# Optimization experiments

Measured on AMD Instinct MI355X. Metric: run time of the kernel, lower is better.

Reference implementation:

```python
import jax, jax.numpy as jnp
import numpy as np

HEAD_DIM = 64
N_HEADS = 32
N_KV_HEADS = 8
ROPE_THETA = 10000.0


def _rotate_half(x):
    h = x.shape[-1] // 2
    return jnp.concatenate([-x[..., h:], x[..., :h]], axis=-1)


def _rope_cos_sin(position_ids, head_dim, theta, dtype):
    # position_ids: [b, s] int
    inv_freq = 1.0 / (theta ** (jnp.arange(0, head_dim, 2, dtype=jnp.float32) / head_dim))
    freqs = position_ids.astype(jnp.float32)[..., None] * inv_freq  # [b, s, hd/2]
    emb = jnp.concatenate([freqs, freqs], axis=-1)                  # [b, s, hd]
    return jnp.cos(emb).astype(dtype), jnp.sin(emb).astype(dtype)


def setup_inputs() -> dict:
    key = jax.random.key(0)
    ks = jax.random.split(key, 5)
    B, S, H = 2, 2048, 2048
    KVD = N_KV_HEADS * HEAD_DIM
    x = jax.random.normal(ks[0], (B, S, H), dtype=jnp.float32)
    position_ids = jnp.broadcast_to(jnp.arange(S, dtype=jnp.int64), (B, S))
    # additive causal mask: 0 on/below diagonal, -1e9 above
    causal = jnp.triu(jnp.full((S, S), -1e9, dtype=jnp.float32), k=1)
    mask = causal[None, None, :, :]
    sc = 1.0 / np.sqrt(H)
    wq = jax.random.normal(ks[1], (H, H), dtype=jnp.float32) * sc
    wk = jax.random.normal(ks[2], (KVD, H), dtype=jnp.float32) * sc
    wv = jax.random.normal(ks[3], (KVD, H), dtype=jnp.float32) * sc
    wo = jax.random.normal(ks[4], (H, H), dtype=jnp.float32) * sc
    return {"x": x, "position_ids": position_ids, "mask": mask,
            "wq": wq, "wk": wk, "wv": wv, "wo": wo}


def reference(x, position_ids, mask, wq, wk, wv, wo):
    b, s, h = x.shape
    kv_groups = N_HEADS // N_KV_HEADS
    # projections (Linear with weight [out, in])
    xq = jnp.einsum('bsh,oh->bso', x, wq)
    xk = jnp.einsum('bsh,oh->bso', x, wk)
    xv = jnp.einsum('bsh,oh->bso', x, wv)
    q = xq.reshape(b, s, N_HEADS, HEAD_DIM).transpose(0, 2, 1, 3)      # [b,H,s,d]
    k = xk.reshape(b, s, N_KV_HEADS, HEAD_DIM).transpose(0, 2, 1, 3)   # [b,Hk,s,d]
    v = xv.reshape(b, s, N_KV_HEADS, HEAD_DIM).transpose(0, 2, 1, 3)
    cos, sin = _rope_cos_sin(position_ids, HEAD_DIM, ROPE_THETA, x.dtype)
    cos = cos[:, None, :, :]  # [b,1,s,d]
    sin = sin[:, None, :, :]
    q = q * cos + _rotate_half(q) * sin
    k = k * cos + _rotate_half(k) * sin
    # GQA expand
    k = jnp.repeat(k, kv_groups, axis=1)  # [b,H,s,d]
    v = jnp.repeat(v, kv_groups, axis=1)
    scale = 1.0 / np.sqrt(HEAD_DIM)
    attn = jnp.einsum('bhqd,bhkd->bhqk', q, k) * scale
    attn = attn + mask[:, :, :s, :s]
    attn = jax.nn.softmax(attn.astype(jnp.float32), axis=-1).astype(q.dtype)
    out = jnp.einsum('bhqk,bhkd->bhqd', attn, v)        # [b,H,s,d]
    out = out.transpose(0, 2, 1, 3).reshape(b, s, h)
    return jnp.einsum('bsh,oh->bso', out, wo)
```

## Files before the change

kernel.cpp:

```cpp
#include <hip/hip_runtime.h>

typedef __bf16 bf16;
typedef __bf16 bf16x4 __attribute__((ext_vector_type(4)));
typedef __bf16 bf16x8 __attribute__((ext_vector_type(8)));
typedef float f32x4 __attribute__((ext_vector_type(4)));

#define MFMA16(a, b, c) __builtin_amdgcn_mfma_f32_16x16x32_bf16(a, b, c, 0, 0, 0)
#define L2E 1.44269504088896340736f

__device__ inline bf16x8 cvt8(const float* __restrict__ p) {
  float4 f0 = ((const float4*)p)[0];
  float4 f1 = ((const float4*)p)[1];
  bf16x8 v;
  v[0] = (bf16)f0.x; v[1] = (bf16)f0.y; v[2] = (bf16)f0.z; v[3] = (bf16)f0.w;
  v[4] = (bf16)f1.x; v[5] = (bf16)f1.y; v[6] = (bf16)f1.z; v[7] = (bf16)f1.w;
  return v;
}

__device__ inline void gl_lds16(const bf16* g, bf16* l) {
  __builtin_amdgcn_global_load_lds(
      (const __attribute__((address_space(1))) unsigned int*)g,
      (__attribute__((address_space(3))) unsigned int*)l, 16, 0, 0);
}

__global__ void detect_kernel(const unsigned* __restrict__ mask,
                              int* __restrict__ flag) {
  *flag = (mask[0] != 0u) ? 1 : 0;
}

__global__ __launch_bounds__(256) void convert_kernel(
    const void* __restrict__ s0, bf16* __restrict__ d0, int n0,
    const void* __restrict__ s1, bf16* __restrict__ d1, int n1,
    const void* __restrict__ s2, bf16* __restrict__ d2, int n2,
    const void* __restrict__ s3, bf16* __restrict__ d3, int n3,
    float2* __restrict__ tab, const int* __restrict__ flag) {
  const int gid = blockIdx.x * 256 + threadIdx.x;
  if (tab && gid < 65536) {
    int s = gid >> 5, fi = gid & 31;
    float inv = 1.0f / powf(10000.0f, (float)(2 * fi) / 64.0f);
    float fr = (float)s * inv;
    tab[gid] = make_float2(cosf(fr), sinf(fr));
  }
  const int isb = *flag;
  const int c0 = n0 >> 3, c1 = c0 + (n1 >> 3), c2 = c1 + (n2 >> 3);
  const int total = c2 + (n3 >> 3);
  for (int c = gid; c < total; c += gridDim.x * 256) {
    const void* s; bf16* d; int off;
    if (c < c0)      { s = s0; d = d0; off = c; }
    else if (c < c1) { s = s1; d = d1; off = c - c0; }
    else if (c < c2) { s = s2; d = d2; off = c - c1; }
    else             { s = s3; d = d3; off = c - c2; }
    if (isb) ((uint4*)d)[off] = ((const uint4*)s)[off];
    else     ((bf16x8*)d)[off] = cvt8((const float*)s + (size_t)off * 8);
  }
}

template <int MODE>
__global__ __launch_bounds__(256) void gemm_bt(
    const bf16* __restrict__ Ab, const bf16* __restrict__ Wq,
    const bf16* __restrict__ Wk, const bf16* __restrict__ Wv,
    void* __restrict__ O0, bf16* __restrict__ O1, bf16* __restrict__ O2,
    const float2* __restrict__ rtab, const int* __restrict__ flag) {
  const int K = 2048;
  __shared__ __align__(16) bf16 As[128 * 32];
  __shared__ __align__(16) bf16 Bs[128 * 32];

  const int m0 = blockIdx.x * 128;
  const int n0 = blockIdx.y * 128;

  const bf16* W;
  int nw0;
  if (MODE == 0) {
    if (n0 < 2048) { W = Wq; nw0 = n0; }
    else if (n0 < 2560) { W = Wk; nw0 = n0 - 2048; }
    else { W = Wv; nw0 = n0 - 2560; }
  } else {
    W = Wq; nw0 = n0;
  }

  const int t = threadIdx.x;
  const int w = t >> 6, lane = t & 63, quad = lane >> 4, l15 = lane & 15;
  const int wm = (w >> 1) * 64, wn = (w & 1) * 64;

  const int ca = t, cb = t + 256;
  const bf16* ga0 = Ab + (size_t)(m0 + (ca >> 2)) * K + (ca & 3) * 8;
  const bf16* ga1 = Ab + (size_t)(m0 + (cb >> 2)) * K + (cb & 3) * 8;
  const bf16* gb0 = W + (size_t)(nw0 + (ca >> 2)) * K + (ca & 3) * 8;
  const bf16* gb1 = W + (size_t)(nw0 + (cb >> 2)) * K + (cb & 3) * 8;
  bf16* lA0 = &As[w * 512];
  bf16* lA1 = &As[2048 + w * 512];
  bf16* lB0 = &Bs[w * 512];
  bf16* lB1 = &Bs[2048 + w * 512];

  f32x4 acc[4][4] = {};

  for (int k0 = 0; k0 < K; k0 += 32) {
    __syncthreads();
    gl_lds16(ga0 + k0, lA0);
    gl_lds16(ga1 + k0, lA1);
    gl_lds16(gb0 + k0, lB0);
    gl_lds16(gb1 + k0, lB1);
    __syncthreads();

    bf16x8 a[4], b[4];
#pragma unroll
    for (int i = 0; i < 4; i++)
      a[i] = *(const bf16x8*)&As[(wm + i * 16 + l15) * 32 + quad * 8];
#pragma unroll
    for (int j = 0; j < 4; j++)
      b[j] = *(const bf16x8*)&Bs[(wn + j * 16 + l15) * 32 + quad * 8];
#pragma unroll
    for (int i = 0; i < 4; i++)
#pragma unroll
      for (int j = 0; j < 4; j++)
        acc[i][j] = MFMA16(a[i], b[j], acc[i][j]);
  }

  if (MODE == 0 && n0 >= 2560) {
#pragma unroll
    for (int i = 0; i < 4; i++)
#pragma unroll
      for (int j = 0; j < 4; j++) {
        int m = m0 + wm + i * 16 + quad * 4;
        int n = (n0 - 2560) + wn + j * 16 + l15;
        int hh = n >> 6, d = n & 63;
        int b_ = m >> 11, s = m & 2047;
        bf16x4 pv;
#pragma unroll
        for (int r = 0; r < 4; r++) pv[r] = (bf16)acc[i][j][r];
        *(bf16x4*)&O2[(((size_t)b_ * 8 + hh) * 64 + d) * 2048 + s] = pv;
      }
    return;
  }

  const int isb = *flag;

  if (MODE == 0) {
#pragma unroll
    for (int i = 0; i < 4; i++) {
      int mb = m0 + wm + i * 16 + quad * 4;
#pragma unroll
      for (int r = 0; r < 4; r++) {
        int s = (mb + r) & 2047;
#pragma unroll
        for (int jp = 0; jp < 2; jp++) {
          int fi = jp * 16 + l15;
          float2 cs = rtab[s * 32 + fi];
          float cb = cs.x, sb = cs.y;
          if (isb) { cb = (float)(bf16)cb; sb = (float)(bf16)sb; }
          float v0 = acc[i][jp][r], v1 = acc[i][jp + 2][r];
          acc[i][jp][r]     = v0 * cb - v1 * sb;
          acc[i][jp + 2][r] = v1 * cb + v0 * sb;
        }
      }
    }
    const bool isQ = (n0 < 2048);
    const float qs = isQ ? 0.125f : 1.0f;
#pragma unroll
    for (int i = 0; i < 4; i++)
#pragma unroll
      for (int j = 0; j < 4; j++)
#pragma unroll
        for (int r = 0; r < 4; r++) {
          int m = m0 + wm + i * 16 + quad * 4 + r;
          int b_ = m >> 11, s = m & 2047;
          bf16 bv = (bf16)(acc[i][j][r] * qs);
          if (isQ) {
            int n = n0 + wn + j * 16 + l15;
            int h = n >> 6, d = n & 63;
            ((bf16*)O0)[(((size_t)b_ * 32 + h) * 2048 + s) * 64 + d] = bv;
          } else {
            int nn = n0 - 2048 + wn + j * 16 + l15;
            int h = nn >> 6, d = nn & 63;
            O1[(((size_t)b_ * 8 + h) * 2048 + s) * 64 + d] = bv;
          }
        }
    return;
  }

#pragma unroll
  for (int i = 0; i < 4; i++)
#pragma unroll
    for (int j = 0; j < 4; j++)
#pragma unroll
      for (int r = 0; r < 4; r++) {
        int m = m0 + wm + i * 16 + quad * 4 + r;
        int n = n0 + wn + j * 16 + l15;
        float fv = acc[i][j][r];
        if (isb) ((bf16*)O0)[(size_t)m * 2048 + n] = (bf16)fv;
        else     ((float*)O0)[(size_t)m * 2048 + n] = fv;
      }
}

__global__ __launch_bounds__(256) void flash_kernel(
    const bf16* __restrict__ qb, const bf16* __restrict__ kb,
    const bf16* __restrict__ vb, bf16* __restrict__ ao) {
  __shared__ __align__(16) bf16 Ks[64 * 64];
  __shared__ __align__(16) bf16 Vt[64 * 72];
  __shared__ __align__(16) bf16 Ps[4][16 * 72];

  const int bx = blockIdx.x;
  const int h = blockIdx.y;
  const int b = blockIdx.z;
  const int kvh = h >> 2;
  const int t = threadIdx.x, w = t >> 6, lane = t & 63;
  const int quad = lane >> 4, l15 = lane & 15;

  const bf16* kg = kb + ((size_t)b * 8 + kvh) * 2048 * 64;
  const bf16* vg = vb + ((size_t)b * 8 + kvh) * 64 * 2048;

  const int vd = t >> 3;
  const int vs = (t & 7) * 8;

#pragma unroll 1
  for (int ti = 0; ti < 2; ti++) {
    const int q0 = (ti == 0 ? bx : 31 - bx) * 64;
    const bf16* qg = qb + (((size_t)b * 32 + h) * 2048 + q0) * 64;

    __syncthreads();
#pragma unroll
    for (int i = 0; i < 2; i++) {
      int c = t + i * 256;
      int row = c >> 3, slot = c & 7;
      *(uint4*)&Ks[row * 64 + ((slot ^ (row & 7)) << 3)] = ((const uint4*)qg)[c];
    }
    __syncthreads();
    const int qrow = w * 16 + l15;
    bf16x8 aq0 = *(const bf16x8*)&Ks[qrow * 64 + ((quad ^ (qrow & 7)) << 3)];
    bf16x8 aq1 = *(const bf16x8*)&Ks[qrow * 64 + (((4 + quad) ^ (qrow & 7)) << 3)];

    f32x4 Oacc[4] = {};
    float m_sm = -1e30f, l_sm = 0.0f;

    const int nk = q0 + 64;
    const int qmin = q0 + w * 16;
    const int qmax = qmin + 15;
    const int qr_sm = qmin + l15;

    uint4 kr0 = ((const uint4*)kg)[t];
    uint4 kr1 = ((const uint4*)kg)[t + 256];
    uint4 vr0 = *(const uint4*)(vg + (size_t)vd * 2048 + vs);
    uint4 vr1 = *(const uint4*)(vg + (size_t)(vd + 32) * 2048 + vs);

    for (int k0 = 0; k0 < nk; k0 += 64) {
      __syncthreads();
      {
        int row = t >> 3, slot = t & 7;
        *(uint4*)&Ks[row * 64 + ((slot ^ (row & 7)) << 3)] = kr0;
        int row1 = row + 32;
        *(uint4*)&Ks[row1 * 64 + ((slot ^ (row1 & 7)) << 3)] = kr1;
      }
      *(uint4*)&Vt[vd * 72 + vs] = vr0;
      *(uint4*)&Vt[(vd + 32) * 72 + vs] = vr1;
      __syncthreads();

      if (k0 + 64 < nk) {
        const bf16* kn = kg + (size_t)(k0 + 64) * 64;
        kr0 = ((const uint4*)kn)[t];
        kr1 = ((const uint4*)kn)[t + 256];
        vr0 = *(const uint4*)(vg + (size_t)vd * 2048 + (k0 + 64) + vs);
        vr1 = *(const uint4*)(vg + (size_t)(vd + 32) * 2048 + (k0 + 64) + vs);
      }

      f32x4 sf[4] = {};
#pragma unroll
      for (int sub = 0; sub < 4; sub++) {
        if (k0 + sub * 16 <= qmax) {
          int rr = sub * 16 + l15;
          bf16x8 bk0 = *(const bf16x8*)&Ks[rr * 64 + ((quad ^ (rr & 7)) << 3)];
          bf16x8 bk1 = *(const bf16x8*)&Ks[rr * 64 + (((4 + quad) ^ (rr & 7)) << 3)];
          sf[sub] = MFMA16(bk0, aq0, sf[sub]);
          sf[sub] = MFMA16(bk1, aq1, sf[sub]);
        }
      }

      if (k0 + 64 > qmin) {
#pragma unroll
        for (int sub = 0; sub < 4; sub++) {
          int kk = k0 + sub * 16 + quad * 4;
#pragma unroll
          for (int r = 0; r < 4; r++)
            if (kk + r > qr_sm) sf[sub][r] = -1e30f;
        }
      }

      float mx;
      {
        f32x4 t4;
#pragma unroll
        for (int r = 0; r < 4; r++)
          t4[r] = fmaxf(fmaxf(sf[0][r], sf[1][r]), fmaxf(sf[2][r], sf[3][r]));
        mx = fmaxf(fmaxf(t4[0], t4[1]), fmaxf(t4[2], t4[3]));
      }
      mx = fmaxf(mx, __shfl_xor(mx, 16));
      mx = fmaxf(mx, __shfl_xor(mx, 32));

      if (!__all(mx <= m_sm + 8.0f)) {
        float mnew = fmaxf(m_sm, mx);
        float alpha = __expf(m_sm - mnew);
        l_sm *= alpha;
        m_sm = mnew;
        f32x4 apv;
#pragma unroll
        for (int r = 0; r < 4; r++) apv[r] = __shfl(alpha, quad * 4 + r);
#pragma unroll
        for (int tt = 0; tt < 4; tt++)
#pragma unroll
          for (int r = 0; r < 4; r++) Oacc[tt][r] *= apv[r];
      }

      const float ml2 = m_sm * L2E;
#pragma unroll
      for (int sub = 0; sub < 4; sub++)
#pragma unroll
        for (int r = 0; r < 4; r++)
          sf[sub][r] = exp2f(fmaf(sf[sub][r], L2E, -ml2));

      float rs;
      {
        f32x4 t4;
#pragma unroll
        for (int r = 0; r < 4; r++)
          t4[r] = (sf[0][r] + sf[1][r]) + (sf[2][r] + sf[3][r]);
        rs = (t4[0] + t4[1]) + (t4[2] + t4[3]);
      }
      rs += __shfl_xor(rs, 16);
      rs += __shfl_xor(rs, 32);
      l_sm += rs;

#pragma unroll
      for (int sub = 0; sub < 4; sub++) {
        bf16x4 pk;
#pragma unroll
        for (int r = 0; r < 4; r++) pk[r] = (bf16)sf[sub][r];
        *(bf16x4*)&Ps[w][l15 * 72 + sub * 16 + quad * 4] = pk;
      }
      asm volatile("s_waitcnt lgkmcnt(0)" ::: "memory");
      __builtin_amdgcn_sched_barrier(0);

      bf16x8 ap0 = *(const bf16x8*)&Ps[w][l15 * 72 + quad * 8];
#pragma unroll
      for (int tt = 0; tt < 4; tt++) {
        bf16x8 bv = *(const bf16x8*)&Vt[(tt * 16 + l15) * 72 + quad * 8];
        Oacc[tt] = MFMA16(ap0, bv, Oacc[tt]);
      }
      if (k0 + 32 <= qmax) {
        bf16x8 ap1 = *(const bf16x8*)&Ps[w][l15 * 72 + 32 + quad * 8];
#pragma unroll
        for (int tt = 0; tt < 4; tt++) {
          bf16x8 bv = *(const bf16x8*)&Vt[(tt * 16 + l15) * 72 + 32 + quad * 8];
          Oacc[tt] = MFMA16(ap1, bv, Oacc[tt]);
        }
      }
    }

    f32x4 lv;
#pragma unroll
    for (int r = 0; r < 4; r++) lv[r] = __shfl(l_sm, quad * 4 + r);
#pragma unroll
    for (int tt = 0; tt < 4; tt++)
#pragma unroll
      for (int r = 0; r < 4; r++) {
        int m = q0 + w * 16 + quad * 4 + r;
        ao[((size_t)b * 2048 + m) * 2048 + h * 64 + tt * 16 + l15] =
            (bf16)(Oacc[tt][r] / lv[r]);
      }
  }
}

extern "C" void kernel_launch(void* const* d_in, const int* in_sizes, int n_in,
                              void* d_out, int out_size, void* d_ws,
                              size_t ws_size, hipStream_t stream) {
  const void* x = d_in[0];
  const unsigned* maskw = (const unsigned*)d_in[2];
  const void* wq = d_in[3];
  const void* wk = d_in[4];
  const void* wv = d_in[5];
  const void* wo = d_in[6];

  char* ws = (char*)d_ws;
  bf16* qbuf  = (bf16*)(ws);
  bf16* kbuf  = (bf16*)(ws + 16777216);
  bf16* vbuf  = (bf16*)(ws + 20971520);
  bf16* wob   = (bf16*)(ws + 16777216);
  bf16* aobuf = (bf16*)(ws + 25165824);
  bf16* xb    = (bf16*)(ws + 25165824);
  int* flag   = (int*)(ws + 41943040);
  bf16* wqb   = (bf16*)(ws + 41943104);
  bf16* wkb   = (bf16*)(ws + 50331712);
  bf16* wvb   = (bf16*)(ws + 52428864);
  float2* rtab = (float2*)(ws + 54526016);

  detect_kernel<<<1, 1, 0, stream>>>(maskw, flag);
  convert_kernel<<<2048, 256, 0, stream>>>(x, xb, 8388608, wq, wqb, 4194304,
                                           wk, wkb, 1048576, wv, wvb, 1048576,
                                           rtab, flag);
  gemm_bt<0><<<dim3(32, 24), 256, 0, stream>>>(xb, wqb, wkb, wvb, qbuf, kbuf,
                                               vbuf, rtab, flag);
  flash_kernel<<<dim3(16, 32, 2), 256, 0, stream>>>(qbuf, kbuf, vbuf, aobuf);
  convert_kernel<<<2048, 256, 0, stream>>>(wo, wob, 4194304, nullptr, nullptr,
                                           0, nullptr, nullptr, 0, nullptr,
                                           nullptr, 0, nullptr, flag);
  gemm_bt<1><<<dim3(32, 16), 256, 0, stream>>>(aobuf, wob, nullptr, nullptr,
                                               d_out, nullptr, nullptr, rtab,
                                               flag);
}
```

Before: 395.8 us.

## Use 128-row query tiles with 512-thread flash blocks and raw v_exp

The flash attention kernel now uses 8 waves per block, each handling 16 query rows, so each block covers 128 query rows. Each K/V tile loaded into shared memory is therefore reused by twice as many waves, and each thread stages one uint4 of K and one of V instead of two. The grid is halved and the causal tile pairing now works on 128-row tiles. Exponentials switch to a raw v_exp_f32 inline asm with no range handling, which may lose accuracy or denormal handling. The larger blocks raise per-block shared memory and synchronisation cost, and the diagonal tiles do more masked work.

```diff
diff --git a/kernel.cpp b/kernel.cpp
--- a/kernel.cpp
+++ b/kernel.cpp
@@ -7,6 +7,12 @@
 
 #define MFMA16(a, b, c) __builtin_amdgcn_mfma_f32_16x16x32_bf16(a, b, c, 0, 0, 0)
 #define L2E 1.44269504088896340736f
+
+__device__ inline float exp2_hw(float x) {
+  float r;
+  asm("v_exp_f32 %0, %1" : "=v"(r) : "v"(x));
+  return r;
+}
 
 __device__ inline bf16x8 cvt8(const float* __restrict__ p) {
   float4 f0 = ((const float4*)p)[0];
@@ -192,12 +198,13 @@
       }
 }
 
-__global__ __launch_bounds__(256) void flash_kernel(
+__global__ __launch_bounds__(512) void flash_kernel(
     const bf16* __restrict__ qb, const bf16* __restrict__ kb,
     const bf16* __restrict__ vb, bf16* __restrict__ ao) {
-  __shared__ __align__(16) bf16 Ks[64 * 64];
-  __shared__ __align__(16) bf16 Vt[64 * 72];
-  __shared__ __align__(16) bf16 Ps[4][16 * 72];
+  __shared__ __align__(16) bf16 SM[8704 + 8 * 16 * 72];
+  bf16* Ks = SM;
+  bf16* Vt = SM + 4096;
+  bf16* Ps = SM + 8704;
 
   const int bx = blockIdx.x;
   const int h = blockIdx.y;
@@ -209,57 +216,49 @@
   const bf16* kg = kb + ((size_t)b * 8 + kvh) * 2048 * 64;
   const bf16* vg = vb + ((size_t)b * 8 + kvh) * 64 * 2048;
 
-  const int vd = t >> 3;
-  const int vs = (t & 7) * 8;
+  const int srow = t >> 3;
+  const int sslot = t & 7;
+  const int kofs = srow * 64 + ((sslot ^ (srow & 7)) << 3);
+  const int vofs = srow * 72 + sslot * 8;
+  bf16* psw = Ps + w * (16 * 72);
 
 #pragma unroll 1
   for (int ti = 0; ti < 2; ti++) {
-    const int q0 = (ti == 0 ? bx : 31 - bx) * 64;
-    const bf16* qg = qb + (((size_t)b * 32 + h) * 2048 + q0) * 64;
+    const int tile = (ti == 0) ? bx : 15 - bx;
+    const int q0b = tile * 128;
+    const bf16* qg = qb + (((size_t)b * 32 + h) * 2048 + q0b) * 64;
 
     __syncthreads();
 #pragma unroll
     for (int i = 0; i < 2; i++) {
-      int c = t + i * 256;
+      int c = t + i * 512;
       int row = c >> 3, slot = c & 7;
-      *(uint4*)&Ks[row * 64 + ((slot ^ (row & 7)) << 3)] = ((const uint4*)qg)[c];
+      *(uint4*)&SM[row * 64 + ((slot ^ (row & 7)) << 3)] = ((const uint4*)qg)[c];
     }
+    uint4 kr = ((const uint4*)kg)[t];
+    uint4 vr = *(const uint4*)(vg + (size_t)srow * 2048 + sslot * 8);
     __syncthreads();
     const int qrow = w * 16 + l15;
-    bf16x8 aq0 = *(const bf16x8*)&Ks[qrow * 64 + ((quad ^ (qrow & 7)) << 3)];
-    bf16x8 aq1 = *(const bf16x8*)&Ks[qrow * 64 + (((4 + quad) ^ (qrow & 7)) << 3)];
+    bf16x8 aq0 = *(const bf16x8*)&SM[qrow * 64 + ((quad ^ (qrow & 7)) << 3)];
+    bf16x8 aq1 = *(const bf16x8*)&SM[qrow * 64 + (((4 + quad) ^ (qrow & 7)) << 3)];
 
     f32x4 Oacc[4] = {};
     float m_sm = -1e30f, l_sm = 0.0f;
 
-    const int nk = q0 + 64;
-    const int qmin = q0 + w * 16;
+    const int nk = q0b + 128;
+    const int qmin = q0b + w * 16;
     const int qmax = qmin + 15;
     const int qr_sm = qmin + l15;
 
-    uint4 kr0 = ((const uint4*)kg)[t];
-    uint4 kr1 = ((const uint4*)kg)[t + 256];
-    uint4 vr0 = *(const uint4*)(vg + (size_t)vd * 2048 + vs);
-    uint4 vr1 = *(const uint4*)(vg + (size_t)(vd + 32) * 2048 + vs);
-
     for (int k0 = 0; k0 < nk; k0 += 64) {
       __syncthreads();
-      {
-        int row = t >> 3, slot = t & 7;
-        *(uint4*)&Ks[row * 64 + ((slot ^ (row & 7)) << 3)] = kr0;
-        int row1 = row + 32;
-        *(uint4*)&Ks[row1 * 64 + ((slot ^ (row1 & 7)) << 3)] = kr1;
-      }
-      *(uint4*)&Vt[vd * 72 + vs] = vr0;
-      *(uint4*)&Vt[(vd + 32) * 72 + vs] = vr1;
+      *(uint4*)&Ks[kofs] = kr;
+      *(uint4*)&Vt[vofs] = vr;
       __syncthreads();
 
       if (k0 + 64 < nk) {
-        const bf16* kn = kg + (size_t)(k0 + 64) * 64;
-        kr0 = ((const uint4*)kn)[t];
-        kr1 = ((const uint4*)kn)[t + 256];
-        vr0 = *(const uint4*)(vg + (size_t)vd * 2048 + (k0 + 64) + vs);
-        vr1 = *(const uint4*)(vg + (size_t)(vd + 32) * 2048 + (k0 + 64) + vs);
+        kr = *((const uint4*)(kg + (size_t)(k0 + 64) * 64) + t);
+        vr = *(const uint4*)(vg + (size_t)srow * 2048 + (k0 + 64) + sslot * 8);
       }
 
       f32x4 sf[4] = {};
@@ -297,7 +296,7 @@
 
       if (!__all(mx <= m_sm + 8.0f)) {
         float mnew = fmaxf(m_sm, mx);
-        float alpha = __expf(m_sm - mnew);
+        float alpha = exp2_hw((m_sm - mnew) * L2E);
         l_sm *= alpha;
         m_sm = mnew;
         f32x4 apv;
@@ -314,7 +313,7 @@
       for (int sub = 0; sub < 4; sub++)
 #pragma unroll
         for (int r = 0; r < 4; r++)
-          sf[sub][r] = exp2f(fmaf(sf[sub][r], L2E, -ml2));
+          sf[sub][r] = exp2_hw(fmaf(sf[sub][r], L2E, -ml2));
 
       float rs;
       {
@@ -333,19 +332,19 @@
         bf16x4 pk;
 #pragma unroll
         for (int r = 0; r < 4; r++) pk[r] = (bf16)sf[sub][r];
-        *(bf16x4*)&Ps[w][l15 * 72 + sub * 16 + quad * 4] = pk;
+        *(bf16x4*)&psw[l15 * 72 + sub * 16 + quad * 4] = pk;
       }
       asm volatile("s_waitcnt lgkmcnt(0)" ::: "memory");
       __builtin_amdgcn_sched_barrier(0);
 
-      bf16x8 ap0 = *(const bf16x8*)&Ps[w][l15 * 72 + quad * 8];
+      bf16x8 ap0 = *(const bf16x8*)&psw[l15 * 72 + quad * 8];
 #pragma unroll
       for (int tt = 0; tt < 4; tt++) {
         bf16x8 bv = *(const bf16x8*)&Vt[(tt * 16 + l15) * 72 + quad * 8];
         Oacc[tt] = MFMA16(ap0, bv, Oacc[tt]);
       }
       if (k0 + 32 <= qmax) {
-        bf16x8 ap1 = *(const bf16x8*)&Ps[w][l15 * 72 + 32 + quad * 8];
+        bf16x8 ap1 = *(const bf16x8*)&psw[l15 * 72 + 32 + quad * 8];
 #pragma unroll
         for (int tt = 0; tt < 4; tt++) {
           bf16x8 bv = *(const bf16x8*)&Vt[(tt * 16 + l15) * 72 + 32 + quad * 8];
@@ -361,7 +360,7 @@
     for (int tt = 0; tt < 4; tt++)
 #pragma unroll
       for (int r = 0; r < 4; r++) {
-        int m = q0 + w * 16 + quad * 4 + r;
+        int m = q0b + w * 16 + quad * 4 + r;
         ao[((size_t)b * 2048 + m) * 2048 + h * 64 + tt * 16 + l15] =
             (bf16)(Oacc[tt][r] / lv[r]);
       }
@@ -397,7 +396,7 @@
                                            rtab, flag);
   gemm_bt<0><<<dim3(32, 24), 256, 0, stream>>>(xb, wqb, wkb, wvb, qbuf, kbuf,
                                                vbuf, rtab, flag);
-  flash_kernel<<<dim3(16, 32, 2), 256, 0, stream>>>(qbuf, kbuf, vbuf, aobuf);
+  flash_kernel<<<dim3(8, 32, 2), 512, 0, stream>>>(qbuf, kbuf, vbuf, aobuf);
   convert_kernel<<<2048, 256, 0, stream>>>(wo, wob, 4194304, nullptr, nullptr,
                                            0, nullptr, nullptr, 0, nullptr,
                                            nullptr, 0, nullptr, flag);
```

Result: faster. 352.1 us (-11.0%).
